# Optimization experiments

Hardware: AMD Instinct MI355X
Metric: run time of the kernel (lower is better)

Reference implementation:

```python
import jax, jax.numpy as jnp
import numpy as np

S = 2048      # seq_len
E = 1024      # embedding_size
H = 16        # attn_head
D = E // H    # per-head dim = 64
EPS = 1e-5


def _layernorm(x, g, b):
    mu = jnp.mean(x, axis=-1, keepdims=True)
    var = jnp.var(x, axis=-1, keepdims=True)
    return (x - mu) * jax.lax.rsqrt(var + EPS) * g + b


def setup_inputs() -> dict:
    key = jax.random.key(0)
    ks = jax.random.split(key, 16)
    s = 1.0 / np.sqrt(E)
    inp = {
        "x_word_emb": jax.random.normal(ks[0], (S, E), jnp.float32),
        "x_pos_emb": jax.random.normal(ks[1], (S, E), jnp.float32),
        # stacked per-head projections: weight [H, E, D], bias [H, D]
        "Wq": jax.random.uniform(ks[2], (H, E, D), jnp.float32, -s, s),
        "bq": jax.random.uniform(ks[3], (H, D), jnp.float32, -s, s),
        "Wk": jax.random.uniform(ks[4], (H, E, D), jnp.float32, -s, s),
        "bk": jax.random.uniform(ks[5], (H, D), jnp.float32, -s, s),
        "Wv": jax.random.uniform(ks[6], (H, E, D), jnp.float32, -s, s),
        "bv": jax.random.uniform(ks[7], (H, D), jnp.float32, -s, s),
        "W0": jax.random.uniform(ks[8], (E, E), jnp.float32, -s, s),
        "b0": jax.random.uniform(ks[9], (E,), jnp.float32, -s, s),
        "g1": jnp.ones((E,), jnp.float32),
        "be1": jnp.zeros((E,), jnp.float32),
        "W1": jax.random.uniform(ks[10], (4 * E, E), jnp.float32, -s, s),
        "b1": jax.random.uniform(ks[11], (4 * E,), jnp.float32, -s, s),
        "W2": jax.random.uniform(ks[12], (E, 4 * E), jnp.float32, -1.0 / np.sqrt(4 * E), 1.0 / np.sqrt(4 * E)),
        "b2": jax.random.uniform(ks[13], (E,), jnp.float32, -1.0 / np.sqrt(4 * E), 1.0 / np.sqrt(4 * E)),
        "g2": jnp.ones((E,), jnp.float32),
        "be2": jnp.zeros((E,), jnp.float32),
    }
    return inp


def reference(x_word_emb, x_pos_emb, Wq, bq, Wk, bk, Wv, bv,
              W0, b0, g1, be1, W1, b1, W2, b2, g2, be2):
    emb = x_word_emb + x_pos_emb                            # [S, E]
    # batched per-head projections (equivalent to the per-head Linear loop)
    q = jnp.einsum('se,hed->hsd', emb, Wq) + bq[:, None, :]  # [H, S, D]
    k = jnp.einsum('se,hed->hsd', emb, Wk) + bk[:, None, :]
    v = jnp.einsum('se,hed->hsd', emb, Wv) + bv[:, None, :]
    scores = jnp.einsum('hsd,htd->hst', q, k)               # [H, S, S]
    # original: F.softmax(z).data -> weights detached (no grad through q/k)
    w = jax.lax.stop_gradient(jax.nn.softmax(scores, axis=-1))
    # NOTE: original scales AFTER softmax@V, not on the logits
    z = jnp.einsum('hst,htd->hsd', w, v) / np.sqrt(D)       # [H, S, D]
    # concat heads along feature dim in head order
    z = jnp.transpose(z, (1, 0, 2)).reshape(S, E)           # [S, E]
    z = z @ W0.T + b0
    out1 = _layernorm(z + emb, g1, be1)
    out2 = jax.nn.relu(out1 @ W1.T + b1)                    # [S, 4E]
    out2 = out2 @ W2.T + b2
    return _layernorm(out1 + out2, g2, be2)
```

## Files before the change

kernel.cpp:

```cpp
#include <hip/hip_runtime.h>

#define SLEN 2048
#define EDIM 1024
#define HNUM 16
#define DDIM 64

typedef unsigned short u16;
typedef unsigned int u32;
typedef __attribute__((ext_vector_type(8))) __bf16 bf16x8;
typedef __attribute__((ext_vector_type(2))) __bf16 bf16x2;
typedef __attribute__((ext_vector_type(4))) float f32x4;

__device__ __forceinline__ u16 f2bf(float f) {
  u32 u = __builtin_bit_cast(u32, f);
  u = (u + 0x7fffu + ((u >> 16) & 1u)) >> 16;
  return (u16)u;
}

__device__ __forceinline__ float bf2f(u16 v) {
  u32 u = ((u32)v) << 16;
  return __builtin_bit_cast(float, u);
}

__device__ __forceinline__ u32 packbf(float a, float b) {
  bf16x2 t; t[0] = (__bf16)a; t[1] = (__bf16)b;
  return __builtin_bit_cast(u32, t);
}

__device__ __forceinline__ void gload_lds16(const void* g, void* l) {
  __builtin_amdgcn_global_load_lds(
      (const __attribute__((address_space(1))) void*)g,
      (__attribute__((address_space(3))) void*)l, 16, 0, 0);
}

__device__ __forceinline__ u32 swz(u32 b) { return b ^ (((b >> 7) & 7u) << 4); }

template<int MODE>
__global__ __launch_bounds__(256, 2) void gemm_bt(
    const u16* __restrict__ A, const u16* __restrict__ Bt,
    const float* __restrict__ bias, const float* __restrict__ add,
    void* __restrict__ outp, int M, int N, int K)
{
  __shared__ __align__(16) u16 As[128 * 64];
  __shared__ __align__(16) u16 Bs[128 * 64];
  const int t = threadIdx.x;
  const int lane = t & 63, wv = t >> 6;
  const int bm = blockIdx.y * 128, bn = blockIdx.x * 128;
  const int wm = (wv >> 1) * 64, wn = (wv & 1) * 64;
  f32x4 acc[4][4] = {};

  const char* Ab = (const char*)A;
  const char* Bb = (const char*)Bt;

  for (int k0 = 0; k0 < K; k0 += 64) {
    __syncthreads();
#pragma unroll
    for (int j = 0; j < 4; ++j) {
      u32 bp = (u32)t * 16u + (u32)j * 4096u;
      u32 L = swz(bp);
      u32 row = L >> 7, colb = L & 127u;
      gload_lds16(Ab + ((size_t)(bm + row) * K + k0) * 2 + colb, (char*)As + bp);
      gload_lds16(Bb + ((size_t)(bn + row) * K + k0) * 2 + colb, (char*)Bs + bp);
    }
    __syncthreads();
#pragma unroll
    for (int ks = 0; ks < 2; ++ks) {
      bf16x8 af[4], bfr[4];
#pragma unroll
      for (int i = 0; i < 4; ++i) {
        u32 ra = (u32)(wm + i * 16 + (lane & 15));
        u32 La = (ra << 7) + (u32)ks * 64u + (u32)(lane >> 4) * 16u;
        af[i] = *(const bf16x8*)((const char*)As + (La ^ ((ra & 7u) << 4)));
        u32 rb = (u32)(wn + i * 16 + (lane & 15));
        u32 Lb = (rb << 7) + (u32)ks * 64u + (u32)(lane >> 4) * 16u;
        bfr[i] = *(const bf16x8*)((const char*)Bs + (Lb ^ ((rb & 7u) << 4)));
      }
#pragma unroll
      for (int mi = 0; mi < 4; ++mi)
#pragma unroll
        for (int ni = 0; ni < 4; ++ni)
          acc[mi][ni] = __builtin_amdgcn_mfma_f32_16x16x32_bf16(af[mi], bfr[ni], acc[mi][ni], 0, 0, 0);
    }
  }

  const int cr = (lane >> 4) * 4, cc = lane & 15;
#pragma unroll
  for (int ni = 0; ni < 4; ++ni) {
    const int col = bn + wn + ni * 16 + cc;
    const float bvv = bias[col];
#pragma unroll
    for (int mi = 0; mi < 4; ++mi) {
#pragma unroll
      for (int r = 0; r < 4; ++r) {
        const int row = bm + wm + mi * 16 + cr + r;
        float v = acc[mi][ni][r] + bvv;
        const size_t idx = (size_t)row * N + col;
        if constexpr (MODE == 0) ((u16*)outp)[idx] = f2bf(v);
        else if constexpr (MODE == 1) ((u16*)outp)[idx] = f2bf(v > 0.f ? v : 0.f);
        else ((float*)outp)[idx] = v + add[idx];
      }
    }
  }
}

template<int MODE>
__global__ __launch_bounds__(256, 4) void gemm_bt64(
    const u16* __restrict__ A, const u16* __restrict__ Bt,
    const float* __restrict__ bias, float* __restrict__ part1,
    void* __restrict__ outp, int M, int N, int lda, int KS)
{
  __shared__ __align__(16) u16 As[64 * 64];
  __shared__ __align__(16) u16 Bs[128 * 64];
  const int t = threadIdx.x;
  const int lane = t & 63, wv = t >> 6;
  const int bm = blockIdx.y * 64, bn = blockIdx.x * 128;
  const int wm = (wv >> 1) * 32, wn = (wv & 1) * 64;
  const int koff = blockIdx.z * KS;
  f32x4 acc[2][4] = {};

  const char* Ab = (const char*)A;
  const char* Bb = (const char*)Bt;

  for (int k0 = koff; k0 < koff + KS; k0 += 64) {
    __syncthreads();
    {
      u32 bp = (u32)t * 16u;
      u32 L = swz(bp);
      u32 row = L >> 7, colb = L & 127u;
      gload_lds16(Ab + ((size_t)(bm + row) * lda + k0) * 2 + colb, (char*)As + bp);
      u32 bp2 = bp + 4096u;
      u32 L2 = swz(bp2);
      u32 row2 = L2 >> 7, colb2 = L2 & 127u;
      gload_lds16(Ab + ((size_t)(bm + row2) * lda + k0) * 2 + colb2, (char*)As + bp2);
    }
#pragma unroll
    for (int j = 0; j < 4; ++j) {
      u32 bp = (u32)t * 16u + (u32)j * 4096u;
      u32 L = swz(bp);
      u32 row = L >> 7, colb = L & 127u;
      gload_lds16(Bb + ((size_t)(bn + row) * lda + k0) * 2 + colb, (char*)Bs + bp);
    }
    __syncthreads();
#pragma unroll
    for (int ks = 0; ks < 2; ++ks) {
      bf16x8 af[2], bfr[4];
#pragma unroll
      for (int i = 0; i < 2; ++i) {
        u32 ra = (u32)(wm + i * 16 + (lane & 15));
        u32 La = (ra << 7) + (u32)ks * 64u + (u32)(lane >> 4) * 16u;
        af[i] = *(const bf16x8*)((const char*)As + (La ^ ((ra & 7u) << 4)));
      }
#pragma unroll
      for (int i = 0; i < 4; ++i) {
        u32 rb = (u32)(wn + i * 16 + (lane & 15));
        u32 Lb = (rb << 7) + (u32)ks * 64u + (u32)(lane >> 4) * 16u;
        bfr[i] = *(const bf16x8*)((const char*)Bs + (Lb ^ ((rb & 7u) << 4)));
      }
#pragma unroll
      for (int mi = 0; mi < 2; ++mi)
#pragma unroll
        for (int ni = 0; ni < 4; ++ni)
          acc[mi][ni] = __builtin_amdgcn_mfma_f32_16x16x32_bf16(af[mi], bfr[ni], acc[mi][ni], 0, 0, 0);
    }
  }

  float* po = (MODE == 3 && blockIdx.z) ? part1 : (float*)outp;
  const int cr = (lane >> 4) * 4, cc = lane & 15;
#pragma unroll
  for (int ni = 0; ni < 4; ++ni) {
    const int col = bn + wn + ni * 16 + cc;
    const float bvv = (MODE == 3) ? 0.f : bias[col];
#pragma unroll
    for (int mi = 0; mi < 2; ++mi) {
#pragma unroll
      for (int r = 0; r < 4; ++r) {
        const int row = bm + wm + mi * 16 + cr + r;
        float v = acc[mi][ni][r] + bvv;
        const size_t idx = (size_t)row * N + col;
        if constexpr (MODE == 0) ((u16*)outp)[idx] = f2bf(v);
        else if constexpr (MODE == 1) ((u16*)outp)[idx] = f2bf(v > 0.f ? v : 0.f);
        else po[idx] = v;
      }
    }
  }
}

__global__ __launch_bounds__(256) void red2_kernel(
    const float4* __restrict__ pA, const float4* __restrict__ pB,
    const float* __restrict__ bias, const float4* __restrict__ add,
    float4* __restrict__ out)
{
  const int i = blockIdx.x * 256 + threadIdx.x;
  float4 a = pA[i], b = pB[i], c = add[i];
  float4 g = ((const float4*)bias)[i & 255];
  float4 o;
  o.x = a.x + b.x + c.x + g.x;
  o.y = a.y + b.y + c.y + g.y;
  o.z = a.z + b.z + c.z + g.z;
  o.w = a.w + b.w + c.w + g.w;
  out[i] = o;
}

__global__ __launch_bounds__(256, 4) void attn_kernel(
    const u16* __restrict__ qkv, const u16* __restrict__ vt,
    u16* __restrict__ zp, float2* __restrict__ mlb)
{
  __shared__ __align__(16) char lds[32768];
  const int t = threadIdx.x, lane = t & 63;
  const int g = lane >> 4, qi = lane & 15;
  const int wv = t >> 6;
  const int h = blockIdx.y;
  const int q0 = blockIdx.x * 64 + wv * 16;
  const int kt0 = blockIdx.z * (SLEN / 128);
  const int ktE = kt0 + SLEN / 128;

  bf16x8 qf[2];
#pragma unroll
  for (int ds = 0; ds < 2; ++ds)
    qf[ds] = *(const bf16x8*)(qkv + (size_t)(q0 + qi) * 3072 + h * 64 + ds * 32 + g * 8);

  const char* kgp[2];
  const char* vgp[2];
  u32 ldo[2];
#pragma unroll
  for (int j = 0; j < 2; ++j) {
    u32 bp = (u32)t * 16u + (u32)j * 4096u;
    u32 L = swz(bp);
    u32 row = L >> 7, colb = L & 127u;
    kgp[j] = (const char*)qkv + ((size_t)row * 3072 + 1024 + h * 64) * 2 + colb;
    vgp[j] = (const char*)vt + ((size_t)(h * 64 + row)) * (SLEN * 2) + colb;
    ldo[j] = bp;
  }

  f32x4 zacc[4] = {};
  float m = -1e30f, l = 0.f;

  {
    char* base = lds;
    size_t ko = (size_t)kt0 * (64 * 3072 * 2);
    int vo = kt0 * 128;
#pragma unroll
    for (int j = 0; j < 2; ++j) {
      gload_lds16(kgp[j] + ko, base + ldo[j]);
      gload_lds16(vgp[j] + vo, base + 8192 + ldo[j]);
    }
  }
  __syncthreads();

  int cur = 0;
  for (int kt = kt0; kt < ktE; ++kt) {
    if (kt + 1 < ktE) {
      char* base = lds + (cur ^ 1) * 16384;
      size_t ko = (size_t)(kt + 1) * (64 * 3072 * 2);
      int vo = (kt + 1) * 128;
#pragma unroll
      for (int j = 0; j < 2; ++j) {
        gload_lds16(kgp[j] + ko, base + ldo[j]);
        gload_lds16(vgp[j] + vo, base + 8192 + ldo[j]);
      }
    }

    const char* Kl = lds + cur * 16384;
    const char* Vl = Kl + 8192;

    float p[4][4];
#pragma unroll
    for (int kcg = 0; kcg < 4; ++kcg) {
      f32x4 s = {};
#pragma unroll
      for (int ds = 0; ds < 2; ++ds) {
        u32 rk = (u32)(kcg * 16 + qi);
        u32 L = (rk << 7) + (u32)ds * 64u + (u32)g * 16u;
        bf16x8 kf = *(const bf16x8*)(Kl + (L ^ ((rk & 7u) << 4)));
        s = __builtin_amdgcn_mfma_f32_16x16x32_bf16(kf, qf[ds], s, 0, 0, 0);
      }
#pragma unroll
      for (int r = 0; r < 4; ++r) p[kcg][r] = s[r];
    }

    float tmax = p[0][0];
#pragma unroll
    for (int kcg = 0; kcg < 4; ++kcg)
#pragma unroll
      for (int r = 0; r < 4; ++r) tmax = fmaxf(tmax, p[kcg][r]);
    tmax = fmaxf(tmax, __shfl_xor(tmax, 16));
    tmax = fmaxf(tmax, __shfl_xor(tmax, 32));

    float newm = fmaxf(m, tmax);
    float scl = __expf(m - newm);
    float psum = 0.f;
    u32 pk[4][2];
#pragma unroll
    for (int kcg = 0; kcg < 4; ++kcg) {
#pragma unroll
      for (int r = 0; r < 4; ++r) {
        float e = __expf(p[kcg][r] - newm);
        p[kcg][r] = e;
        psum += e;
      }
      pk[kcg][0] = packbf(p[kcg][0], p[kcg][1]);
      pk[kcg][1] = packbf(p[kcg][2], p[kcg][3]);
    }
    psum += __shfl_xor(psum, 16);
    psum += __shfl_xor(psum, 32);
    l = l * scl + psum;
    m = newm;
#pragma unroll
    for (int ni = 0; ni < 4; ++ni)
#pragma unroll
      for (int r = 0; r < 4; ++r) zacc[ni][r] *= scl;

#pragma unroll
    for (int ks = 0; ks < 2; ++ks) {
      u32 w[4];
#pragma unroll
      for (int wi = 0; wi < 4; ++wi) {
        const int src = qi + 16 * (2 * (g & 1) + (wi >> 1));
        u32 wa = (u32)__shfl((int)pk[2 * ks][wi & 1], src);
        u32 wb = (u32)__shfl((int)pk[2 * ks + 1][wi & 1], src);
        w[wi] = (g & 2) ? wb : wa;
      }
      uint4 wp = {w[0], w[1], w[2], w[3]};
      bf16x8 pb = __builtin_bit_cast(bf16x8, wp);
#pragma unroll
      for (int ni = 0; ni < 4; ++ni) {
        u32 rv = (u32)(ni * 16 + qi);
        u32 L = (rv << 7) + (u32)ks * 64u + (u32)g * 16u;
        bf16x8 vf = *(const bf16x8*)(Vl + (L ^ ((rv & 7u) << 4)));
        zacc[ni] = __builtin_amdgcn_mfma_f32_16x16x32_bf16(vf, pb, zacc[ni], 0, 0, 0);
      }
    }

    __syncthreads();
    cur ^= 1;
  }

  const int bid = (h * 32 + blockIdx.x) * 2 + blockIdx.z;
  u16* zb = zp + (size_t)bid * 4096;
#pragma unroll
  for (int ni = 0; ni < 4; ++ni) {
    u32 a = packbf(zacc[ni][0], zacc[ni][1]);
    u32 b = packbf(zacc[ni][2], zacc[ni][3]);
    uint2 st = {a, b};
    *(uint2*)(zb + (size_t)(wv * 16 + qi) * 64 + ni * 16 + g * 4) = st;
  }
  if (g == 0) mlb[(size_t)bid * 64 + wv * 16 + qi] = make_float2(m, l);
}

__global__ __launch_bounds__(256) void comb_kernel(
    const u16* __restrict__ zp, const float2* __restrict__ mlb, u16* __restrict__ zcat)
{
  const int flat = blockIdx.x * 256 + threadIdx.x;
  const int d4 = flat & 15;
  const int q = (flat >> 4) & 2047;
  const int h = flat >> 15;
  const int qt = q >> 6, qr = q & 63;
  const size_t pb = (size_t)(h * 32 + qt) * 2;
  const size_t base = pb * 4096 + (size_t)qr * 64 + d4 * 4;
  uint2 a = *(const uint2*)(zp + base);
  uint2 b = *(const uint2*)(zp + base + 4096);
  float2 ml0 = mlb[pb * 64 + qr];
  float2 ml1 = mlb[(pb + 1) * 64 + qr];
  const float M = fmaxf(ml0.x, ml1.x);
  const float e0 = __expf(ml0.x - M), e1 = __expf(ml1.x - M);
  const float s = 0.125f / (e0 * ml0.y + e1 * ml1.y);
  float o0 = (e0 * bf2f((u16)(a.x & 0xffff)) + e1 * bf2f((u16)(b.x & 0xffff))) * s;
  float o1 = (e0 * bf2f((u16)(a.x >> 16))   + e1 * bf2f((u16)(b.x >> 16))) * s;
  float o2 = (e0 * bf2f((u16)(a.y & 0xffff)) + e1 * bf2f((u16)(b.y & 0xffff))) * s;
  float o3 = (e0 * bf2f((u16)(a.y >> 16))   + e1 * bf2f((u16)(b.y >> 16))) * s;
  uint2 st;
  st.x = (u32)f2bf(o0) | ((u32)f2bf(o1) << 16);
  st.y = (u32)f2bf(o2) | ((u32)f2bf(o3) << 16);
  *(uint2*)(zcat + (size_t)q * EDIM + h * 64 + d4 * 4) = st;
}

__global__ __launch_bounds__(256) void ln_kernel(
    const float* __restrict__ in, const float* __restrict__ g, const float* __restrict__ b,
    float* __restrict__ outf, u16* __restrict__ outb)
{
  const int row = blockIdx.x, t = threadIdx.x;
  const float4* rp = (const float4*)(in + (size_t)row * EDIM);
  float4 x = rp[t];
  float s = x.x + x.y + x.z + x.w;
  float sq = x.x * x.x + x.y * x.y + x.z * x.z + x.w * x.w;
#pragma unroll
  for (int m = 1; m < 64; m <<= 1) { s += __shfl_xor(s, m); sq += __shfl_xor(sq, m); }
  __shared__ float red[8];
  const int wv = t >> 6, lane = t & 63;
  if (lane == 0) { red[wv] = s; red[4 + wv] = sq; }
  __syncthreads();
  s = red[0] + red[1] + red[2] + red[3];
  sq = red[4] + red[5] + red[6] + red[7];
  const float mu = s * (1.f / EDIM);
  const float rs = rsqrtf(sq * (1.f / EDIM) - mu * mu + 1e-5f);
  float4 gg = ((const float4*)g)[t];
  float4 bb = ((const float4*)b)[t];
  float4 y;
  y.x = (x.x - mu) * rs * gg.x + bb.x;
  y.y = (x.y - mu) * rs * gg.y + bb.y;
  y.z = (x.z - mu) * rs * gg.z + bb.z;
  y.w = (x.w - mu) * rs * gg.w + bb.w;
  if (outf) ((float4*)(outf + (size_t)row * EDIM))[t] = y;
  if (outb) {
    uint2 pkv;
    pkv.x = (u32)f2bf(y.x) | ((u32)f2bf(y.y) << 16);
    pkv.y = (u32)f2bf(y.z) | ((u32)f2bf(y.w) << 16);
    ((uint2*)(outb + (size_t)row * EDIM))[t] = pkv;
  }
}

__global__ void emb_kernel(const float4* __restrict__ a, const float4* __restrict__ b,
                           float4* __restrict__ ef, uint2* __restrict__ eb)
{
  const int i = blockIdx.x * 256 + threadIdx.x;
  float4 x = a[i], y = b[i];
  float4 e; e.x = x.x + y.x; e.y = x.y + y.y; e.z = x.z + y.z; e.w = x.w + y.w;
  ef[i] = e;
  uint2 pk;
  pk.x = (u32)f2bf(e.x) | ((u32)f2bf(e.y) << 16);
  pk.y = (u32)f2bf(e.z) | ((u32)f2bf(e.w) << 16);
  eb[i] = pk;
}

__global__ void cvt_kernel(const float4* __restrict__ in, uint2* __restrict__ out, int n4)
{
  const int i = blockIdx.x * 256 + threadIdx.x;
  if (i >= n4) return;
  float4 x = in[i];
  uint2 pk;
  pk.x = (u32)f2bf(x.x) | ((u32)f2bf(x.y) << 16);
  pk.y = (u32)f2bf(x.z) | ((u32)f2bf(x.w) << 16);
  out[i] = pk;
}

__global__ void bias3_kernel(const float* __restrict__ bq, const float* __restrict__ bk,
                             const float* __restrict__ bv, float* __restrict__ o)
{
  const int i = blockIdx.x * 256 + threadIdx.x;
  if (i >= 3072) return;
  o[i] = i < 1024 ? bq[i] : (i < 2048 ? bk[i - 1024] : bv[i - 2048]);
}

__global__ __launch_bounds__(256) void wqkv_kernel(
    const float* __restrict__ Wq, const float* __restrict__ Wk, const float* __restrict__ Wv,
    u16* __restrict__ outw)
{
  __shared__ float tile[64][65];
  const int et = blockIdx.x, h = blockIdx.y, wsel = blockIdx.z;
  const float* W = wsel == 0 ? Wq : (wsel == 1 ? Wk : Wv);
  const float* src = W + ((size_t)h * EDIM + et * 64) * DDIM;
  const int t = threadIdx.x;
#pragma unroll
  for (int it = 0; it < 4; ++it) {
    int fi = (t + it * 256) * 4;
    float4 v = *(const float4*)(src + fi);
    int e = fi >> 6, d = fi & 63;
    tile[e][d] = v.x; tile[e][d + 1] = v.y; tile[e][d + 2] = v.z; tile[e][d + 3] = v.w;
  }
  __syncthreads();
  const int d = t >> 2, ec = (t & 3) * 16;
  u16* dst = outw + ((size_t)(wsel * HNUM + h) * 64 + d) * EDIM + et * 64 + ec;
#pragma unroll
  for (int i = 0; i < 16; i += 2) {
    u32 p = (u32)f2bf(tile[ec + i][d]) | ((u32)f2bf(tile[ec + i + 1][d]) << 16);
    *(u32*)(dst + i) = p;
  }
}

__global__ __launch_bounds__(256) void vt_kernel(const u16* __restrict__ qkv, u16* __restrict__ vt)
{
  __shared__ __align__(16) u16 tile[64][80];
  const int st = blockIdx.x, h = blockIdx.y, t = threadIdx.x;
  const int sr = t >> 2, dc = (t & 3) * 16;
  const u16* src = qkv + (size_t)(st * 64 + sr) * 3072 + 2048 + h * 64 + dc;
  *(uint4*)&tile[sr][dc] = *(const uint4*)src;
  *(uint4*)&tile[sr][dc + 8] = *(const uint4*)(src + 8);
  __syncthreads();
  const int d = t >> 2, sc = (t & 3) * 16;
  u16* dst = vt + ((size_t)h * 64 + d) * SLEN + st * 64 + sc;
#pragma unroll
  for (int i = 0; i < 16; i += 2) {
    u32 p = (u32)tile[sc + i][d] | ((u32)tile[sc + i + 1][d] << 16);
    *(u32*)(dst + i) = p;
  }
}

extern "C" void kernel_launch(void* const* d_in, const int* in_sizes, int n_in,
                              void* d_out, int out_size, void* d_ws, size_t ws_size,
                              hipStream_t stream) {
  const float* xw  = (const float*)d_in[0];
  const float* xp  = (const float*)d_in[1];
  const float* Wq  = (const float*)d_in[2];
  const float* bq  = (const float*)d_in[3];
  const float* Wk  = (const float*)d_in[4];
  const float* bk  = (const float*)d_in[5];
  const float* Wv  = (const float*)d_in[6];
  const float* bv  = (const float*)d_in[7];
  const float* W0  = (const float*)d_in[8];
  const float* b0  = (const float*)d_in[9];
  const float* g1  = (const float*)d_in[10];
  const float* be1 = (const float*)d_in[11];
  const float* W1  = (const float*)d_in[12];
  const float* b1  = (const float*)d_in[13];
  const float* W2  = (const float*)d_in[14];
  const float* b2  = (const float*)d_in[15];
  const float* g2  = (const float*)d_in[16];
  const float* be2 = (const float*)d_in[17];
  float* out = (float*)d_out;
  char* ws = (char*)d_ws;

  const size_t MB = 1ull << 20;
  float* embf32 = (float*)(ws + 0);
  u16*   embf16 = (u16*)(ws + 8 * MB);
  u16*   zcat   = (u16*)(ws + 8 * MB);
  float* res2   = (float*)(ws + 8 * MB);
  u16*   Wqkvt  = (u16*)(ws + 12 * MB);
  u16*   h1     = (u16*)(ws + 12 * MB);
  u16*   QKV    = (u16*)(ws + 18 * MB);
  float* w0pA   = (float*)(ws + 18 * MB);
  float* w0pB   = (float*)(ws + 26 * MB);
  u16*   Vt     = (u16*)(ws + 30 * MB);
  u16*   zp     = (u16*)(ws + 34 * MB);
  float2* mlb   = (float2*)(ws + 42 * MB);
  float* res1   = (float*)(ws + 34 * MB);
  float* out1f  = (float*)(ws + 34 * MB);
  u16*   out1b  = (u16*)(ws + 28 * MB);
  u16*   W0b    = (u16*)(ws + 46 * MB);
  u16*   W1b    = (u16*)(ws + 48 * MB);
  u16*   W2b    = (u16*)(ws + 56 * MB);
  float* w2pA   = (float*)(ws + 0);
  float* w2pB   = (float*)(ws + 48 * MB);
  float* bias3  = (float*)(ws + 64 * MB);

  emb_kernel<<<2048, 256, 0, stream>>>((const float4*)xw, (const float4*)xp,
                                       (float4*)embf32, (uint2*)embf16);
  cvt_kernel<<<1024, 256, 0, stream>>>((const float4*)W0, (uint2*)W0b, 1024 * 1024 / 4);
  cvt_kernel<<<4096, 256, 0, stream>>>((const float4*)W1, (uint2*)W1b, 4096 * 1024 / 4);
  cvt_kernel<<<4096, 256, 0, stream>>>((const float4*)W2, (uint2*)W2b, 1024 * 4096 / 4);
  bias3_kernel<<<12, 256, 0, stream>>>(bq, bk, bv, bias3);
  wqkv_kernel<<<dim3(16, 16, 3), 256, 0, stream>>>(Wq, Wk, Wv, Wqkvt);

  gemm_bt64<0><<<dim3(3072 / 128, 2048 / 64, 1), 256, 0, stream>>>(
      embf16, Wqkvt, bias3, nullptr, QKV, SLEN, 3072, 1024, 1024);

  vt_kernel<<<dim3(32, 16), 256, 0, stream>>>(QKV, Vt);

  attn_kernel<<<dim3(SLEN / 64, HNUM, 2), 256, 0, stream>>>(QKV, Vt, zp, mlb);
  comb_kernel<<<2048, 256, 0, stream>>>(zp, mlb, zcat);

  gemm_bt64<3><<<dim3(1024 / 128, 2048 / 64, 2), 256, 0, stream>>>(
      zcat, W0b, nullptr, w0pB, w0pA, SLEN, 1024, 1024, 512);
  red2_kernel<<<2048, 256, 0, stream>>>((const float4*)w0pA, (const float4*)w0pB,
                                        b0, (const float4*)embf32, (float4*)res1);

  ln_kernel<<<SLEN, 256, 0, stream>>>(res1, g1, be1, out1f, out1b);

  gemm_bt<1><<<dim3(4096 / 128, 2048 / 128), 256, 0, stream>>>(
      out1b, W1b, b1, nullptr, h1, SLEN, 4096, 1024);

  gemm_bt64<3><<<dim3(1024 / 128, 2048 / 64, 2), 256, 0, stream>>>(
      h1, W2b, nullptr, w2pB, w2pA, SLEN, 1024, 4096, 2048);
  red2_kernel<<<2048, 256, 0, stream>>>((const float4*)w2pA, (const float4*)w2pB,
                                        b2, (const float4*)out1f, (float4*)res2);

  ln_kernel<<<SLEN, 256, 0, stream>>>(res2, g2, be2, out, nullptr);
}
```

Before: 187.2 us.

## Use 32x32 MFMA attention with 3-way KV split and fuse reduction into layernorm

```diff
diff --git a/kernel.cpp b/kernel.cpp
--- a/kernel.cpp
+++ b/kernel.cpp
@@ -10,6 +10,7 @@
 typedef __attribute__((ext_vector_type(8))) __bf16 bf16x8;
 typedef __attribute__((ext_vector_type(2))) __bf16 bf16x2;
 typedef __attribute__((ext_vector_type(4))) float f32x4;
+typedef __attribute__((ext_vector_type(16))) float f32x16;
 
 __device__ __forceinline__ u16 f2bf(float f) {
   u32 u = __builtin_bit_cast(u32, f);
@@ -185,39 +186,23 @@
   }
 }
 
-__global__ __launch_bounds__(256) void red2_kernel(
-    const float4* __restrict__ pA, const float4* __restrict__ pB,
-    const float* __restrict__ bias, const float4* __restrict__ add,
-    float4* __restrict__ out)
-{
-  const int i = blockIdx.x * 256 + threadIdx.x;
-  float4 a = pA[i], b = pB[i], c = add[i];
-  float4 g = ((const float4*)bias)[i & 255];
-  float4 o;
-  o.x = a.x + b.x + c.x + g.x;
-  o.y = a.y + b.y + c.y + g.y;
-  o.z = a.z + b.z + c.z + g.z;
-  o.w = a.w + b.w + c.w + g.w;
-  out[i] = o;
-}
-
 __global__ __launch_bounds__(256, 4) void attn_kernel(
     const u16* __restrict__ qkv, const u16* __restrict__ vt,
     u16* __restrict__ zp, float2* __restrict__ mlb)
 {
   __shared__ __align__(16) char lds[32768];
   const int t = threadIdx.x, lane = t & 63;
-  const int g = lane >> 4, qi = lane & 15;
+  const int q31 = lane & 31, hi = lane >> 5;
   const int wv = t >> 6;
   const int h = blockIdx.y;
-  const int q0 = blockIdx.x * 64 + wv * 16;
-  const int kt0 = blockIdx.z * (SLEN / 128);
-  const int ktE = kt0 + SLEN / 128;
-
-  bf16x8 qf[2];
-#pragma unroll
-  for (int ds = 0; ds < 2; ++ds)
-    qf[ds] = *(const bf16x8*)(qkv + (size_t)(q0 + qi) * 3072 + h * 64 + ds * 32 + g * 8);
+  const int qrow = blockIdx.x * 128 + wv * 32 + q31;
+  const int kt0 = blockIdx.z * 12;
+  const int cnt = (blockIdx.z == 2) ? 8 : 12;
+
+  bf16x8 qf[4];
+#pragma unroll
+  for (int ds = 0; ds < 4; ++ds)
+    qf[ds] = *(const bf16x8*)(qkv + (size_t)qrow * 3072 + h * 64 + ds * 16 + hi * 8);
 
   const char* kgp[2];
   const char* vgp[2];
@@ -232,24 +217,24 @@
     ldo[j] = bp;
   }
 
-  f32x4 zacc[4] = {};
+  f32x16 zacc[2] = {};
   float m = -1e30f, l = 0.f;
 
   {
-    char* base = lds;
     size_t ko = (size_t)kt0 * (64 * 3072 * 2);
     int vo = kt0 * 128;
 #pragma unroll
     for (int j = 0; j < 2; ++j) {
-      gload_lds16(kgp[j] + ko, base + ldo[j]);
-      gload_lds16(vgp[j] + vo, base + 8192 + ldo[j]);
+      gload_lds16(kgp[j] + ko, lds + ldo[j]);
+      gload_lds16(vgp[j] + vo, lds + 8192 + ldo[j]);
     }
   }
   __syncthreads();
 
   int cur = 0;
-  for (int kt = kt0; kt < ktE; ++kt) {
-    if (kt + 1 < ktE) {
+  for (int it = 0; it < cnt; ++it) {
+    const int kt = kt0 + it;
+    if (it + 1 < cnt) {
       char* base = lds + (cur ^ 1) * 16384;
       size_t ko = (size_t)(kt + 1) * (64 * 3072 * 2);
       int vo = (kt + 1) * 128;
@@ -263,88 +248,75 @@
     const char* Kl = lds + cur * 16384;
     const char* Vl = Kl + 8192;
 
-    float p[4][4];
-#pragma unroll
-    for (int kcg = 0; kcg < 4; ++kcg) {
-      f32x4 s = {};
-#pragma unroll
-      for (int ds = 0; ds < 2; ++ds) {
-        u32 rk = (u32)(kcg * 16 + qi);
-        u32 L = (rk << 7) + (u32)ds * 64u + (u32)g * 16u;
+#pragma unroll
+    for (int kh = 0; kh < 2; ++kh) {
+      f32x16 p = {};
+#pragma unroll
+      for (int ds = 0; ds < 4; ++ds) {
+        u32 rk = (u32)(kh * 32 + q31);
+        u32 L = (rk << 7) + (u32)ds * 32u + (u32)hi * 16u;
         bf16x8 kf = *(const bf16x8*)(Kl + (L ^ ((rk & 7u) << 4)));
-        s = __builtin_amdgcn_mfma_f32_16x16x32_bf16(kf, qf[ds], s, 0, 0, 0);
-      }
-#pragma unroll
-      for (int r = 0; r < 4; ++r) p[kcg][r] = s[r];
-    }
-
-    float tmax = p[0][0];
-#pragma unroll
-    for (int kcg = 0; kcg < 4; ++kcg)
-#pragma unroll
-      for (int r = 0; r < 4; ++r) tmax = fmaxf(tmax, p[kcg][r]);
-    tmax = fmaxf(tmax, __shfl_xor(tmax, 16));
-    tmax = fmaxf(tmax, __shfl_xor(tmax, 32));
-
-    float newm = fmaxf(m, tmax);
-    float scl = __expf(m - newm);
-    float psum = 0.f;
-    u32 pk[4][2];
-#pragma unroll
-    for (int kcg = 0; kcg < 4; ++kcg) {
-#pragma unroll
-      for (int r = 0; r < 4; ++r) {
-        float e = __expf(p[kcg][r] - newm);
-        p[kcg][r] = e;
-        psum += e;
-      }
-      pk[kcg][0] = packbf(p[kcg][0], p[kcg][1]);
-      pk[kcg][1] = packbf(p[kcg][2], p[kcg][3]);
-    }
-    psum += __shfl_xor(psum, 16);
-    psum += __shfl_xor(psum, 32);
-    l = l * scl + psum;
-    m = newm;
-#pragma unroll
-    for (int ni = 0; ni < 4; ++ni)
-#pragma unroll
-      for (int r = 0; r < 4; ++r) zacc[ni][r] *= scl;
-
-#pragma unroll
-    for (int ks = 0; ks < 2; ++ks) {
-      u32 w[4];
-#pragma unroll
-      for (int wi = 0; wi < 4; ++wi) {
-        const int src = qi + 16 * (2 * (g & 1) + (wi >> 1));
-        u32 wa = (u32)__shfl((int)pk[2 * ks][wi & 1], src);
-        u32 wb = (u32)__shfl((int)pk[2 * ks + 1][wi & 1], src);
-        w[wi] = (g & 2) ? wb : wa;
-      }
-      uint4 wp = {w[0], w[1], w[2], w[3]};
-      bf16x8 pb = __builtin_bit_cast(bf16x8, wp);
-#pragma unroll
-      for (int ni = 0; ni < 4; ++ni) {
-        u32 rv = (u32)(ni * 16 + qi);
-        u32 L = (rv << 7) + (u32)ks * 64u + (u32)g * 16u;
-        bf16x8 vf = *(const bf16x8*)(Vl + (L ^ ((rv & 7u) << 4)));
-        zacc[ni] = __builtin_amdgcn_mfma_f32_16x16x32_bf16(vf, pb, zacc[ni], 0, 0, 0);
-      }
-    }
-
+        p = __builtin_amdgcn_mfma_f32_32x32x16_bf16(kf, qf[ds], p, 0, 0, 0);
+      }
+
+      float tmax = p[0];
+#pragma unroll
+      for (int r = 1; r < 16; ++r) tmax = fmaxf(tmax, p[r]);
+      tmax = fmaxf(tmax, __shfl_xor(tmax, 32));
+      if (!__all(tmax <= m)) {
+        float newm = fmaxf(m, tmax);
+        float scl = __expf(m - newm);
+        l *= scl;
+#pragma unroll
+        for (int r = 0; r < 16; ++r) { zacc[0][r] *= scl; zacc[1][r] *= scl; }
+        m = newm;
+      }
+      float psum = 0.f;
+      u32 w[8];
+#pragma unroll
+      for (int j = 0; j < 8; ++j) {
+        float e0 = __expf(p[2 * j] - m);
+        float e1 = __expf(p[2 * j + 1] - m);
+        psum += e0 + e1;
+        w[j] = packbf(e0, e1);
+      }
+      psum += __shfl_xor(psum, 32);
+      l += psum;
+
+#pragma unroll
+      for (int ktl = 0; ktl < 2; ++ktl) {
+        u32 A0 = w[4 * ktl + 0], B0 = w[4 * ktl + 2];
+        asm volatile("v_permlane32_swap_b32 %0, %1" : "+v"(A0), "+v"(B0));
+        u32 A1 = w[4 * ktl + 1], B1 = w[4 * ktl + 3];
+        asm volatile("v_permlane32_swap_b32 %0, %1" : "+v"(A1), "+v"(B1));
+        uint4 pw = {A0, A1, B0, B1};
+        bf16x8 pf = __builtin_bit_cast(bf16x8, pw);
+#pragma unroll
+        for (int dh = 0; dh < 2; ++dh) {
+          u32 rv = (u32)(dh * 32 + q31);
+          u32 L = (rv << 7) + (u32)(kh * 64 + ktl * 32) + (u32)hi * 16u;
+          bf16x8 vf = *(const bf16x8*)(Vl + (L ^ ((rv & 7u) << 4)));
+          zacc[dh] = __builtin_amdgcn_mfma_f32_32x32x16_bf16(vf, pf, zacc[dh], 0, 0, 0);
+        }
+      }
+    }
     __syncthreads();
     cur ^= 1;
   }
 
-  const int bid = (h * 32 + blockIdx.x) * 2 + blockIdx.z;
-  u16* zb = zp + (size_t)bid * 4096;
-#pragma unroll
-  for (int ni = 0; ni < 4; ++ni) {
-    u32 a = packbf(zacc[ni][0], zacc[ni][1]);
-    u32 b = packbf(zacc[ni][2], zacc[ni][3]);
-    uint2 st = {a, b};
-    *(uint2*)(zb + (size_t)(wv * 16 + qi) * 64 + ni * 16 + g * 4) = st;
-  }
-  if (g == 0) mlb[(size_t)bid * 64 + wv * 16 + qi] = make_float2(m, l);
+  const int bid = (h * 16 + blockIdx.x) * 3 + blockIdx.z;
+  u16* zb = zp + (size_t)bid * 8192 + (size_t)(wv * 32 + q31) * 64;
+#pragma unroll
+  for (int dh = 0; dh < 2; ++dh)
+#pragma unroll
+    for (int g = 0; g < 4; ++g) {
+      int d0 = dh * 32 + g * 8 + hi * 4;
+      uint2 st;
+      st.x = packbf(zacc[dh][4 * g + 0], zacc[dh][4 * g + 1]);
+      st.y = packbf(zacc[dh][4 * g + 2], zacc[dh][4 * g + 3]);
+      *(uint2*)(zb + d0) = st;
+    }
+  if (hi == 0) mlb[(size_t)bid * 128 + wv * 32 + q31] = make_float2(m, l);
 }
 
 __global__ __launch_bounds__(256) void comb_kernel(
@@ -354,37 +326,47 @@
   const int d4 = flat & 15;
   const int q = (flat >> 4) & 2047;
   const int h = flat >> 15;
-  const int qt = q >> 6, qr = q & 63;
-  const size_t pb = (size_t)(h * 32 + qt) * 2;
-  const size_t base = pb * 4096 + (size_t)qr * 64 + d4 * 4;
+  const int qt = q >> 7, qr = q & 127;
+  const size_t pb = (size_t)(h * 16 + qt) * 3;
+  const size_t base = pb * 8192 + (size_t)qr * 64 + d4 * 4;
   uint2 a = *(const uint2*)(zp + base);
-  uint2 b = *(const uint2*)(zp + base + 4096);
-  float2 ml0 = mlb[pb * 64 + qr];
-  float2 ml1 = mlb[(pb + 1) * 64 + qr];
-  const float M = fmaxf(ml0.x, ml1.x);
-  const float e0 = __expf(ml0.x - M), e1 = __expf(ml1.x - M);
-  const float s = 0.125f / (e0 * ml0.y + e1 * ml1.y);
-  float o0 = (e0 * bf2f((u16)(a.x & 0xffff)) + e1 * bf2f((u16)(b.x & 0xffff))) * s;
-  float o1 = (e0 * bf2f((u16)(a.x >> 16))   + e1 * bf2f((u16)(b.x >> 16))) * s;
-  float o2 = (e0 * bf2f((u16)(a.y & 0xffff)) + e1 * bf2f((u16)(b.y & 0xffff))) * s;
-  float o3 = (e0 * bf2f((u16)(a.y >> 16))   + e1 * bf2f((u16)(b.y >> 16))) * s;
+  uint2 b = *(const uint2*)(zp + base + 8192);
+  uint2 c = *(const uint2*)(zp + base + 16384);
+  float2 ml0 = mlb[pb * 128 + qr];
+  float2 ml1 = mlb[(pb + 1) * 128 + qr];
+  float2 ml2 = mlb[(pb + 2) * 128 + qr];
+  const float M = fmaxf(fmaxf(ml0.x, ml1.x), ml2.x);
+  const float e0 = __expf(ml0.x - M), e1 = __expf(ml1.x - M), e2 = __expf(ml2.x - M);
+  const float s = 0.125f / (e0 * ml0.y + e1 * ml1.y + e2 * ml2.y);
+  float o0 = (e0 * bf2f((u16)(a.x & 0xffff)) + e1 * bf2f((u16)(b.x & 0xffff)) + e2 * bf2f((u16)(c.x & 0xffff))) * s;
+  float o1 = (e0 * bf2f((u16)(a.x >> 16))   + e1 * bf2f((u16)(b.x >> 16))   + e2 * bf2f((u16)(c.x >> 16))) * s;
+  float o2 = (e0 * bf2f((u16)(a.y & 0xffff)) + e1 * bf2f((u16)(b.y & 0xffff)) + e2 * bf2f((u16)(c.y & 0xffff))) * s;
+  float o3 = (e0 * bf2f((u16)(a.y >> 16))   + e1 * bf2f((u16)(b.y >> 16))   + e2 * bf2f((u16)(c.y >> 16))) * s;
   uint2 st;
   st.x = (u32)f2bf(o0) | ((u32)f2bf(o1) << 16);
   st.y = (u32)f2bf(o2) | ((u32)f2bf(o3) << 16);
   *(uint2*)(zcat + (size_t)q * EDIM + h * 64 + d4 * 4) = st;
 }
 
-__global__ __launch_bounds__(256) void ln_kernel(
-    const float* __restrict__ in, const float* __restrict__ g, const float* __restrict__ b,
+__global__ __launch_bounds__(256) void lnred_kernel(
+    const float4* __restrict__ pA, const float4* __restrict__ pB,
+    const float* __restrict__ bias, const float4* __restrict__ add,
+    const float* __restrict__ g, const float* __restrict__ b,
     float* __restrict__ outf, u16* __restrict__ outb)
 {
   const int row = blockIdx.x, t = threadIdx.x;
-  const float4* rp = (const float4*)(in + (size_t)row * EDIM);
-  float4 x = rp[t];
+  const int i = row * 256 + t;
+  float4 a = pA[i], p2 = pB[i], c = add[i];
+  float4 bs = ((const float4*)bias)[t];
+  float4 x;
+  x.x = a.x + p2.x + c.x + bs.x;
+  x.y = a.y + p2.y + c.y + bs.y;
+  x.z = a.z + p2.z + c.z + bs.z;
+  x.w = a.w + p2.w + c.w + bs.w;
   float s = x.x + x.y + x.z + x.w;
   float sq = x.x * x.x + x.y * x.y + x.z * x.z + x.w * x.w;
 #pragma unroll
-  for (int m = 1; m < 64; m <<= 1) { s += __shfl_xor(s, m); sq += __shfl_xor(sq, m); }
+  for (int msk = 1; msk < 64; msk <<= 1) { s += __shfl_xor(s, msk); sq += __shfl_xor(sq, msk); }
   __shared__ float red[8];
   const int wv = t >> 6, lane = t & 63;
   if (lane == 0) { red[wv] = s; red[4 + wv] = sq; }
@@ -513,23 +495,21 @@
   float* embf32 = (float*)(ws + 0);
   u16*   embf16 = (u16*)(ws + 8 * MB);
   u16*   zcat   = (u16*)(ws + 8 * MB);
-  float* res2   = (float*)(ws + 8 * MB);
+  u16*   out1b  = (u16*)(ws + 8 * MB);
   u16*   Wqkvt  = (u16*)(ws + 12 * MB);
+  float2* mlb   = (float2*)(ws + 12 * MB);
   u16*   h1     = (u16*)(ws + 12 * MB);
   u16*   QKV    = (u16*)(ws + 18 * MB);
   float* w0pA   = (float*)(ws + 18 * MB);
   float* w0pB   = (float*)(ws + 26 * MB);
   u16*   Vt     = (u16*)(ws + 30 * MB);
   u16*   zp     = (u16*)(ws + 34 * MB);
-  float2* mlb   = (float2*)(ws + 42 * MB);
-  float* res1   = (float*)(ws + 34 * MB);
   float* out1f  = (float*)(ws + 34 * MB);
-  u16*   out1b  = (u16*)(ws + 28 * MB);
   u16*   W0b    = (u16*)(ws + 46 * MB);
   u16*   W1b    = (u16*)(ws + 48 * MB);
   u16*   W2b    = (u16*)(ws + 56 * MB);
   float* w2pA   = (float*)(ws + 0);
-  float* w2pB   = (float*)(ws + 48 * MB);
+  float* w2pB   = (float*)(ws + 42 * MB);
   float* bias3  = (float*)(ws + 64 * MB);
 
   emb_kernel<<<2048, 256, 0, stream>>>((const float4*)xw, (const float4*)xp,
@@ -545,23 +525,19 @@
 
   vt_kernel<<<dim3(32, 16), 256, 0, stream>>>(QKV, Vt);
 
-  attn_kernel<<<dim3(SLEN / 64, HNUM, 2), 256, 0, stream>>>(QKV, Vt, zp, mlb);
+  attn_kernel<<<dim3(SLEN / 128, HNUM, 3), 256, 0, stream>>>(QKV, Vt, zp, mlb);
   comb_kernel<<<2048, 256, 0, stream>>>(zp, mlb, zcat);
 
   gemm_bt64<3><<<dim3(1024 / 128, 2048 / 64, 2), 256, 0, stream>>>(
       zcat, W0b, nullptr, w0pB, w0pA, SLEN, 1024, 1024, 512);
-  red2_kernel<<<2048, 256, 0, stream>>>((const float4*)w0pA, (const float4*)w0pB,
-                                        b0, (const float4*)embf32, (float4*)res1);
-
-  ln_kernel<<<SLEN, 256, 0, stream>>>(res1, g1, be1, out1f, out1b);
+  lnred_kernel<<<SLEN, 256, 0, stream>>>((const float4*)w0pA, (const float4*)w0pB,
+                                         b0, (const float4*)embf32, g1, be1, out1f, out1b);
 
   gemm_bt<1><<<dim3(4096 / 128, 2048 / 128), 256, 0, stream>>>(
       out1b, W1b, b1, nullptr, h1, SLEN, 4096, 1024);
 
   gemm_bt64<3><<<dim3(1024 / 128, 2048 / 64, 2), 256, 0, stream>>>(
       h1, W2b, nullptr, w2pB, w2pA, SLEN, 1024, 4096, 2048);
-  red2_kernel<<<2048, 256, 0, stream>>>((const float4*)w2pA, (const float4*)w2pB,
-                                        b2, (const float4*)out1f, (float4*)res2);
-
-  ln_kernel<<<SLEN, 256, 0, stream>>>(res2, g2, be2, out, nullptr);
-}
+  lnred_kernel<<<SLEN, 256, 0, stream>>>((const float4*)w2pA, (const float4*)w2pB,
+                                         b2, (const float4*)out1f, g2, be2, out, nullptr);
+}
```

New measurement: 169.3 us. 1.11x faster.
